# Performance work log

Hardware: AMD Instinct MI355X
Metric: run time of the kernel (lower is better)

## Reference

```python
import jax, jax.numpy as jnp
import numpy as np

N_NODES = 50000
N_EDGES = 800000
DIM = 128


def setup_inputs() -> dict:
    key = jax.random.key(0)
    k_x, k_e, k_w1, k_w2 = jax.random.split(key, 4)
    x = jax.random.normal(k_x, (N_NODES, DIM), dtype=jnp.float32)
    edge_index = jax.random.randint(k_e, (2, N_EDGES), 0, N_NODES, dtype=jnp.int64)
    scale = 1.0 / np.sqrt(DIM)
    W1 = jax.random.normal(k_w1, (DIM, DIM), dtype=jnp.float32) * scale
    b1 = jnp.zeros((DIM,), dtype=jnp.float32)
    W2 = jax.random.normal(k_w2, (DIM, DIM), dtype=jnp.float32) * scale
    b2 = jnp.zeros((DIM,), dtype=jnp.float32)
    return {"x": x, "edge_index": edge_index, "W1": W1, "b1": b1, "W2": W2, "b2": b2}


def _gcn_conv(x, W, b, src, dst, n_nodes):
    """PyG GCNConv: D^{-1/2}(A+I)D^{-1/2} (x @ W) + b, self-loops added."""
    h = x @ W  # [N, D]
    ones = jnp.ones(src.shape[0], dtype=h.dtype)
    # degree of A+I, counting incoming edges at target nodes plus self-loop
    deg = jax.ops.segment_sum(ones, dst, num_segments=n_nodes) + 1.0
    dinv = jax.lax.rsqrt(deg)  # [N]
    norm = dinv[src] * dinv[dst]  # [E]
    msgs = h[src] * norm[:, None]  # [E, D] gather (memory-bound)
    agg = jax.ops.segment_sum(msgs, dst, num_segments=n_nodes)  # scatter-add
    agg = agg + h * (dinv * dinv)[:, None]  # self-loop contribution
    return agg + b


def reference(x, edge_index, W1, b1, W2, b2):
    src, dst = edge_index[0], edge_index[1]
    n = x.shape[0]
    identity = x
    out = jax.nn.relu(_gcn_conv(x, W1, b1, src, dst, n))
    out = _gcn_conv(out, W2, b2, src, dst, n)
    return jax.nn.relu(out + identity)
```

## Files before the change

kernel.cpp:

```cpp
#include <hip/hip_runtime.h>

#define N_NODES 50000
#define N_EDGES 800000
#define DIM 128
#define NB 391
#define CAP 2560
#define NCH 7
#define BIN_CHUNK 4096
#define BIN_BLOCKS 196
#define GEMM_TILES 782
#define AGG_TILES 3125

typedef unsigned int uint;
typedef unsigned short ushort;
typedef __attribute__((ext_vector_type(8))) __bf16 bf16x8;
typedef __attribute__((ext_vector_type(4))) float f32x4;

__device__ __forceinline__ uint f2bf(float f) {
    uint u = __float_as_uint(f);
    return (u + 0x7FFFu + ((u >> 16) & 1u)) >> 16;
}
__device__ __forceinline__ float2 bf2f2(uint u) {
    return make_float2(__uint_as_float(u << 16), __uint_as_float(u & 0xFFFF0000u));
}


__global__ __launch_bounds__(256) void prep_kernel(const float* __restrict__ W1,
                                                   const float* __restrict__ W2,
                                                   uint* __restrict__ Wt1,
                                                   uint* __restrict__ Wt2,
                                                   int* __restrict__ bincursor) {
    int idx = blockIdx.x * 256 + threadIdx.x;
    if (idx < 16384) {
        const float* W = (idx < 8192) ? W1 : W2;
        uint* Wt = (idx < 8192) ? Wt1 : Wt2;
        int i = idx & 8191;
        int n = i >> 6, k2 = i & 63;
        Wt[i] = f2bf(W[(2 * k2) * DIM + n]) | (f2bf(W[(2 * k2 + 1) * DIM + n]) << 16);
    } else {
        int b = idx - 16384;
        if (b < NB) bincursor[b] = b * CAP;
    }
}


__device__ __forceinline__ void gemm_tile64(const float* __restrict__ X,
                                            const uint* __restrict__ Wt, int base,
                                            uint* __restrict__ Hout) {
    int t = threadIdx.x;
    int wv = t >> 6;
    int l = t & 63;
    int col = l & 15;
    int g = l >> 4;
    int grow = base + wv * 16 + col;
    int ar = grow > N_NODES - 1 ? N_NODES - 1 : grow;

    bf16x8 af[4];
    const float4* Xr = (const float4*)(X + (size_t)ar * DIM);
#pragma unroll
    for (int kk = 0; kk < 4; ++kk) {
        float4 x0 = Xr[kk * 8 + g * 2];
        float4 x1 = Xr[kk * 8 + g * 2 + 1];
        uint4 p;
        p.x = f2bf(x0.x) | (f2bf(x0.y) << 16);
        p.y = f2bf(x0.z) | (f2bf(x0.w) << 16);
        p.z = f2bf(x1.x) | (f2bf(x1.y) << 16);
        p.w = f2bf(x1.z) | (f2bf(x1.w) << 16);
        af[kk] = __builtin_bit_cast(bf16x8, p);
    }

    const uint4* Wr = (const uint4*)Wt;
    f32x4 acc[8];
#pragma unroll
    for (int n = 0; n < 8; ++n) acc[n] = (f32x4){0.f, 0.f, 0.f, 0.f};

#pragma unroll
    for (int n = 0; n < 8; ++n) {
        const uint4* wrow = Wr + (size_t)(n * 16 + col) * 16;
#pragma unroll
        for (int kk = 0; kk < 4; ++kk) {
            bf16x8 bf = __builtin_bit_cast(bf16x8, wrow[kk * 4 + g]);
            acc[n] = __builtin_amdgcn_mfma_f32_16x16x32_bf16(af[kk], bf, acc[n], 0, 0, 0);
        }
    }

#pragma unroll
    for (int j = 0; j < 4; ++j) {
        int row = base + wv * 16 + g * 4 + j;
        if (row < N_NODES) {
            ushort* hrow = (ushort*)(Hout + (size_t)row * 64);
#pragma unroll
            for (int n = 0; n < 8; ++n) hrow[n * 16 + col] = (ushort)f2bf(acc[n][j]);
        }
    }
}


__device__ __forceinline__ void gemm_tile16_lds(const uint* __restrict__ sB,
                                                const uint* __restrict__ Wt,
                                                const float* __restrict__ dinv, int base,
                                                uint* __restrict__ Hout) {
    int t = threadIdx.x;
    int wv = t >> 6;
    int l = t & 63;
    int col = l & 15;
    int g = l >> 4;
    int lr = col;

    bf16x8 af[4];
#pragma unroll
    for (int kk = 0; kk < 4; ++kk) {
        int ui = lr * 64 + ((kk * 16 + g * 4) ^ ((lr & 7) << 2));
        af[kk] = __builtin_bit_cast(bf16x8, *(const uint4*)&sB[ui]);
    }

    const uint4* Wr = (const uint4*)Wt;
    f32x4 acc[2];
#pragma unroll
    for (int nn = 0; nn < 2; ++nn) acc[nn] = (f32x4){0.f, 0.f, 0.f, 0.f};

#pragma unroll
    for (int nn = 0; nn < 2; ++nn) {
        int n = wv * 2 + nn;
        const uint4* wrow = Wr + (size_t)(n * 16 + col) * 16;
#pragma unroll
        for (int kk = 0; kk < 4; ++kk) {
            bf16x8 bf = __builtin_bit_cast(bf16x8, wrow[kk * 4 + g]);
            acc[nn] = __builtin_amdgcn_mfma_f32_16x16x32_bf16(af[kk], bf, acc[nn], 0, 0, 0);
        }
    }

#pragma unroll
    for (int j = 0; j < 4; ++j) {
        int row = base + g * 4 + j;
        float di = dinv[row];
        ushort* hrow = (ushort*)(Hout + (size_t)row * 64);
#pragma unroll
        for (int nn = 0; nn < 2; ++nn) {
            int n = wv * 2 + nn;
            hrow[n * 16 + col] = (ushort)f2bf(acc[nn][j] * di);
        }
    }
}


__global__ __launch_bounds__(256) void bin_gemm1_kernel(const int* __restrict__ ei,
                                                        int* __restrict__ bincursor,
                                                        uint* __restrict__ pairs,
                                                        const float* __restrict__ x,
                                                        const uint* __restrict__ Wt1,
                                                        uint* __restrict__ Hs) {
    if (blockIdx.x >= BIN_BLOCKS) {
        gemm_tile64(x, Wt1, (blockIdx.x - BIN_BLOCKS) * 64, Hs);
        return;
    }
    __shared__ int lh[NB];
    __shared__ int lbase[NB];
    int t = threadIdx.x;
    int eb = blockIdx.x * BIN_CHUNK;

    for (int b = t; b < NB; b += 256) lh[b] = 0;
    __syncthreads();

    int s_reg[16], d_reg[16];
#pragma unroll
    for (int i = 0; i < 16; ++i) {
        int e = eb + i * 256 + t;
        if (e < N_EDGES) {
            s_reg[i] = ei[e];
            d_reg[i] = ei[N_EDGES + e];
            atomicAdd(&lh[d_reg[i] >> 7], 1);
        } else {
            d_reg[i] = -1;
        }
    }
    __syncthreads();

    for (int b = t; b < NB; b += 256) {
        int c = lh[b];
        lbase[b] = c ? atomicAdd(&bincursor[b], c) : 0;
    }
    __syncthreads();
    for (int b = t; b < NB; b += 256) lh[b] = 0;
    __syncthreads();

#pragma unroll
    for (int i = 0; i < 16; ++i) {
        int d = d_reg[i];
        if (d >= 0) {
            int bin = d >> 7;
            int r = atomicAdd(&lh[bin], 1);
            pairs[lbase[bin] + r] = ((uint)s_reg[i] << 7) | (uint)(d & 127);
        }
    }
}


__global__ __launch_bounds__(256) void fill2_kernel(const uint* __restrict__ pairs,
                                                    const int* __restrict__ bincursor,
                                                    int* __restrict__ rowbeg,
                                                    int* __restrict__ rowend,
                                                    float* __restrict__ dinv,
                                                    int* __restrict__ csr_src) {
    __shared__ int cnt[128 * 8];
    __shared__ int nsum[128];
    __shared__ int nbase[128];
    int t = threadIdx.x;
    int blk = blockIdx.x;
    int bs = blk * CAP;
    int be = bincursor[blk];

    for (int i = t; i < 128 * 8; i += 256) cnt[i] = 0;
    __syncthreads();

    for (int p = bs + t; p < be; p += 256) {
        uint pr = pairs[p];
        atomicAdd(&cnt[(pr & 127u) * 8 + (pr >> 20)], 1);
    }
    __syncthreads();

    if (t < 128) {
        int s = 0;
#pragma unroll
        for (int c = 0; c < NCH; ++c) s += cnt[t * 8 + c];
        nsum[t] = s;
        nbase[t] = s;
    }
    __syncthreads();
#pragma unroll
    for (int off = 1; off < 128; off <<= 1) {
        int v = (t < 128 && t >= off) ? nbase[t - off] : 0;
        __syncthreads();
        if (t < 128) nbase[t] += v;
        __syncthreads();
    }

    if (t < 128) {
        int ex = nbase[t] - nsum[t];
        int node = blk * 128 + t;
        if (node < N_NODES) {
            rowbeg[node] = bs + ex;
            rowend[node] = bs + nbase[t];
            dinv[node] = rsqrtf((float)nsum[t] + 1.0f);
        }
        int run = ex;
#pragma unroll
        for (int c = 0; c < NCH; ++c) {
            int v = cnt[t * 8 + c];
            cnt[t * 8 + c] = run;
            run += v;
        }
    }
    __syncthreads();

    for (int p = bs + t; p < be; p += 256) {
        uint pr = pairs[p];
        int r = atomicAdd(&cnt[(pr & 127u) * 8 + (pr >> 20)], 1);
        csr_src[bs + r] = (int)(pr >> 7);
    }
}


template <bool DSRC>
__device__ __forceinline__ void agg_node(const int* __restrict__ rowbeg,
                                         const int* __restrict__ rowend,
                                         const int* __restrict__ csr_src,
                                         const uint* __restrict__ Hs,
                                         const float* __restrict__ dinv,
                                         const float* __restrict__ bias, int node, int li,
                                         float r[8]) {
    int beg = rowbeg[node];
    int end = rowend[node];
    float di = dinv[node];

    const uint4* H4 = (const uint4*)Hs;
    float a0, a1, a2, a3, a4, a5, a6, a7;
    {
        uint4 su = H4[(size_t)node * 16 + li];
        float2 v0 = bf2f2(su.x), v1 = bf2f2(su.y), v2 = bf2f2(su.z), v3 = bf2f2(su.w);
        float sf = DSRC ? di : 1.0f;
        a0 = sf * v0.x; a1 = sf * v0.y; a2 = sf * v1.x; a3 = sf * v1.y;
        a4 = sf * v2.x; a5 = sf * v2.y; a6 = sf * v3.x; a7 = sf * v3.y;
    }

#define ADDF8(u, f)                                                               \
    {                                                                             \
        float2 v0 = bf2f2(u.x), v1 = bf2f2(u.y), v2 = bf2f2(u.z), v3 = bf2f2(u.w);\
        a0 += f * v0.x; a1 += f * v0.y; a2 += f * v1.x; a3 += f * v1.y;           \
        a4 += f * v2.x; a5 += f * v2.y; a6 += f * v3.x; a7 += f * v3.y;           \
    }

    int e = beg;
    for (; e + 7 < end; e += 8) {
        int s[8];
#pragma unroll
        for (int i = 0; i < 8; ++i) s[i] = csr_src[e + i];
        uint4 u[8];
#pragma unroll
        for (int i = 0; i < 8; ++i) u[i] = H4[(size_t)s[i] * 16 + li];
        float f[8];
#pragma unroll
        for (int i = 0; i < 8; ++i) f[i] = DSRC ? dinv[s[i]] : 1.0f;
#pragma unroll
        for (int i = 0; i < 8; ++i) ADDF8(u[i], f[i]);
    }
    if (e + 3 < end) {
        int s[4];
#pragma unroll
        for (int i = 0; i < 4; ++i) s[i] = csr_src[e + i];
        uint4 u[4];
#pragma unroll
        for (int i = 0; i < 4; ++i) u[i] = H4[(size_t)s[i] * 16 + li];
        float f[4];
#pragma unroll
        for (int i = 0; i < 4; ++i) f[i] = DSRC ? dinv[s[i]] : 1.0f;
#pragma unroll
        for (int i = 0; i < 4; ++i) ADDF8(u[i], f[i]);
        e += 4;
    }
    for (; e < end; ++e) {
        int s = csr_src[e];
        uint4 u = H4[(size_t)s * 16 + li];
        float f = DSRC ? dinv[s] : 1.0f;
        ADDF8(u, f);
    }
#undef ADDF8

    const float4* B4 = (const float4*)bias;
    float4 bb0 = B4[li * 2], bb1 = B4[li * 2 + 1];
    r[0] = a0 * di + bb0.x; r[1] = a1 * di + bb0.y;
    r[2] = a2 * di + bb0.z; r[3] = a3 * di + bb0.w;
    r[4] = a4 * di + bb1.x; r[5] = a5 * di + bb1.y;
    r[6] = a6 * di + bb1.z; r[7] = a7 * di + bb1.w;
}


__global__ __launch_bounds__(256) void aggemm_kernel(const int* __restrict__ rowbeg,
                                                     const int* __restrict__ rowend,
                                                     const int* __restrict__ csr_src,
                                                     const uint* __restrict__ Hs,
                                                     const float* __restrict__ dinv,
                                                     const float* __restrict__ b1,
                                                     const uint* __restrict__ Wt2,
                                                     uint* __restrict__ Hs2) {
    __shared__ uint sB[16 * 64];
    int t = threadIdx.x;
    int wv = t >> 6;
    int lane = t & 63;
    int grp = lane >> 4;
    int li = lane & 15;
    int base = blockIdx.x * 16;

    {
        int row = wv * 4 + grp;
        int node = base + row;
        float r[8];
        agg_node<true>(rowbeg, rowend, csr_src, Hs, dinv, b1, node, li, r);
        uint4 o;
        o.x = f2bf(fmaxf(r[0], 0.f)) | (f2bf(fmaxf(r[1], 0.f)) << 16);
        o.y = f2bf(fmaxf(r[2], 0.f)) | (f2bf(fmaxf(r[3], 0.f)) << 16);
        o.z = f2bf(fmaxf(r[4], 0.f)) | (f2bf(fmaxf(r[5], 0.f)) << 16);
        o.w = f2bf(fmaxf(r[6], 0.f)) | (f2bf(fmaxf(r[7], 0.f)) << 16);
        int ui = row * 64 + ((li * 4) ^ ((row & 7) << 2));
        *(uint4*)&sB[ui] = o;
    }
    __syncthreads();

    gemm_tile16_lds(sB, Wt2, dinv, base, Hs2);
}


__global__ __launch_bounds__(256) void agg2_kernel(const int* __restrict__ rowbeg,
                                                   const int* __restrict__ rowend,
                                                   const int* __restrict__ csr_src,
                                                   const uint* __restrict__ Hs2,
                                                   const float* __restrict__ dinv,
                                                   const float* __restrict__ b2,
                                                   const float* __restrict__ resid,
                                                   float* __restrict__ out) {
    int wave = (int)((blockIdx.x * (size_t)blockDim.x + threadIdx.x) >> 6);
    int lane = threadIdx.x & 63;
    int grp = lane >> 4;
    int li = lane & 15;
    int node = wave * 4 + grp;

    float r[8];
    agg_node<false>(rowbeg, rowend, csr_src, Hs2, dinv, b2, node, li, r);

    const float4* R4 = (const float4*)(resid + (size_t)node * DIM);
    float4 x0 = R4[li * 2], x1 = R4[li * 2 + 1];
    r[0] += x0.x; r[1] += x0.y; r[2] += x0.z; r[3] += x0.w;
    r[4] += x1.x; r[5] += x1.y; r[6] += x1.z; r[7] += x1.w;

    float4* O4 = (float4*)(out + (size_t)node * DIM);
    O4[li * 2] = make_float4(fmaxf(r[0], 0.f), fmaxf(r[1], 0.f), fmaxf(r[2], 0.f),
                             fmaxf(r[3], 0.f));
    O4[li * 2 + 1] = make_float4(fmaxf(r[4], 0.f), fmaxf(r[5], 0.f), fmaxf(r[6], 0.f),
                                 fmaxf(r[7], 0.f));
}


extern "C" void kernel_launch(void* const* d_in, const int* in_sizes, int n_in,
                              void* d_out, int out_size, void* d_ws, size_t ws_size,
                              hipStream_t stream) {
    const float* x = (const float*)d_in[0];
    const int* edge_index = (const int*)d_in[1];
    const float* W1 = (const float*)d_in[2];
    const float* b1 = (const float*)d_in[3];
    const float* W2 = (const float*)d_in[4];
    const float* b2 = (const float*)d_in[5];
    float* out = (float*)d_out;

    char* ws = (char*)d_ws;
    int*   bincursor = (int*)(ws + 0);
    float* dinv      = (float*)(ws + (64 << 10));
    int*   rowbeg    = (int*)(ws + (320 << 10));
    int*   rowend    = (int*)(ws + (576 << 10));
    int*   csr_src   = (int*)(ws + (1 << 20));
    uint*  pairs     = (uint*)(ws + (6 << 20));
    uint*  Hs        = (uint*)(ws + (11 << 20));
    uint*  Hs2       = (uint*)(ws + (24 << 20));
    uint*  Wt1       = (uint*)(ws + (37 << 20));
    uint*  Wt2       = (uint*)(ws + (37 << 20) + (64 << 10));

    prep_kernel<<<66, 256, 0, stream>>>(W1, W2, Wt1, Wt2, bincursor);
    bin_gemm1_kernel<<<BIN_BLOCKS + GEMM_TILES, 256, 0, stream>>>(edge_index, bincursor, pairs,
                                                                  x, Wt1, Hs);
    fill2_kernel<<<NB, 256, 0, stream>>>(pairs, bincursor, rowbeg, rowend, dinv, csr_src);
    aggemm_kernel<<<AGG_TILES, 256, 0, stream>>>(rowbeg, rowend, csr_src, Hs, dinv, b1, Wt2,
                                                 Hs2);
    agg2_kernel<<<3125, 256, 0, stream>>>(rowbeg, rowend, csr_src, Hs2, dinv, b2, x, out);
}
```

Baseline: 120.9 us.

## Make aggregate+GEMM2 wave-local, removing block barrier with per-wave LDS strips

Each wave now aggregates its own 4 nodes, stages them in a private padded LDS strip, and runs the second GEMM on just those 4 rows (rows replicated across the 16-row MFMA A operand), so the block-wide __syncthreads is gone. Waves no longer wait for the slowest neighbor's irregular-degree aggregation before starting MFMA work. In exchange, each wave does all 8 output column tiles with 4x redundant A rows, loading the full W2 per wave and quadrupling MFMA work, and only a quarter of lanes write results.

Result: slower. 152.3 us (+26.0%).

```diff
diff --git a/kernel.cpp b/kernel.cpp
--- a/kernel.cpp
+++ b/kernel.cpp
@@ -96,54 +96,6 @@
 }
 
 
-__device__ __forceinline__ void gemm_tile16_lds(const uint* __restrict__ sB,
-                                                const uint* __restrict__ Wt,
-                                                const float* __restrict__ dinv, int base,
-                                                uint* __restrict__ Hout) {
-    int t = threadIdx.x;
-    int wv = t >> 6;
-    int l = t & 63;
-    int col = l & 15;
-    int g = l >> 4;
-    int lr = col;
-
-    bf16x8 af[4];
-#pragma unroll
-    for (int kk = 0; kk < 4; ++kk) {
-        int ui = lr * 64 + ((kk * 16 + g * 4) ^ ((lr & 7) << 2));
-        af[kk] = __builtin_bit_cast(bf16x8, *(const uint4*)&sB[ui]);
-    }
-
-    const uint4* Wr = (const uint4*)Wt;
-    f32x4 acc[2];
-#pragma unroll
-    for (int nn = 0; nn < 2; ++nn) acc[nn] = (f32x4){0.f, 0.f, 0.f, 0.f};
-
-#pragma unroll
-    for (int nn = 0; nn < 2; ++nn) {
-        int n = wv * 2 + nn;
-        const uint4* wrow = Wr + (size_t)(n * 16 + col) * 16;
-#pragma unroll
-        for (int kk = 0; kk < 4; ++kk) {
-            bf16x8 bf = __builtin_bit_cast(bf16x8, wrow[kk * 4 + g]);
-            acc[nn] = __builtin_amdgcn_mfma_f32_16x16x32_bf16(af[kk], bf, acc[nn], 0, 0, 0);
-        }
-    }
-
-#pragma unroll
-    for (int j = 0; j < 4; ++j) {
-        int row = base + g * 4 + j;
-        float di = dinv[row];
-        ushort* hrow = (ushort*)(Hout + (size_t)row * 64);
-#pragma unroll
-        for (int nn = 0; nn < 2; ++nn) {
-            int n = wv * 2 + nn;
-            hrow[n * 16 + col] = (ushort)f2bf(acc[nn][j] * di);
-        }
-    }
-}
-
-
 __global__ __launch_bounds__(256) void bin_gemm1_kernel(const int* __restrict__ ei,
                                                         int* __restrict__ bincursor,
                                                         uint* __restrict__ pairs,
@@ -343,30 +295,59 @@
                                                      const float* __restrict__ b1,
                                                      const uint* __restrict__ Wt2,
                                                      uint* __restrict__ Hs2) {
-    __shared__ uint sB[16 * 64];
+    __shared__ uint sB[4][4 * 68];
     int t = threadIdx.x;
     int wv = t >> 6;
     int lane = t & 63;
     int grp = lane >> 4;
     int li = lane & 15;
     int base = blockIdx.x * 16;
-
-    {
-        int row = wv * 4 + grp;
-        int node = base + row;
-        float r[8];
-        agg_node<true>(rowbeg, rowend, csr_src, Hs, dinv, b1, node, li, r);
-        uint4 o;
-        o.x = f2bf(fmaxf(r[0], 0.f)) | (f2bf(fmaxf(r[1], 0.f)) << 16);
-        o.y = f2bf(fmaxf(r[2], 0.f)) | (f2bf(fmaxf(r[3], 0.f)) << 16);
-        o.z = f2bf(fmaxf(r[4], 0.f)) | (f2bf(fmaxf(r[5], 0.f)) << 16);
-        o.w = f2bf(fmaxf(r[6], 0.f)) | (f2bf(fmaxf(r[7], 0.f)) << 16);
-        int ui = row * 64 + ((li * 4) ^ ((row & 7) << 2));
-        *(uint4*)&sB[ui] = o;
-    }
-    __syncthreads();
-
-    gemm_tile16_lds(sB, Wt2, dinv, base, Hs2);
+    int node = base + wv * 4 + grp;
+
+    float r[8];
+    agg_node<true>(rowbeg, rowend, csr_src, Hs, dinv, b1, node, li, r);
+
+    uint4 o;
+    o.x = f2bf(fmaxf(r[0], 0.f)) | (f2bf(fmaxf(r[1], 0.f)) << 16);
+    o.y = f2bf(fmaxf(r[2], 0.f)) | (f2bf(fmaxf(r[3], 0.f)) << 16);
+    o.z = f2bf(fmaxf(r[4], 0.f)) | (f2bf(fmaxf(r[5], 0.f)) << 16);
+    o.w = f2bf(fmaxf(r[6], 0.f)) | (f2bf(fmaxf(r[7], 0.f)) << 16);
+    uint* strip = sB[wv];
+    *(uint4*)&strip[grp * 68 + li * 4] = o;
+    asm volatile("s_waitcnt lgkmcnt(0)" ::: "memory");
+
+    bf16x8 af[4];
+#pragma unroll
+    for (int kk = 0; kk < 4; ++kk) {
+        af[kk] = __builtin_bit_cast(
+            bf16x8, *(const uint4*)&strip[(lane & 3) * 68 + kk * 16 + grp * 4]);
+    }
+
+    float di4[4];
+    if (grp == 0) {
+#pragma unroll
+        for (int j = 0; j < 4; ++j) di4[j] = dinv[base + wv * 4 + j];
+    }
+
+    const uint4* Wr = (const uint4*)Wt2;
+#pragma unroll
+    for (int n = 0; n < 8; ++n) {
+        f32x4 acc = (f32x4){0.f, 0.f, 0.f, 0.f};
+        const uint4* wrow = Wr + (size_t)(n * 16 + li) * 16;
+#pragma unroll
+        for (int kk = 0; kk < 4; ++kk) {
+            bf16x8 bf = __builtin_bit_cast(bf16x8, wrow[kk * 4 + grp]);
+            acc = __builtin_amdgcn_mfma_f32_16x16x32_bf16(af[kk], bf, acc, 0, 0, 0);
+        }
+        if (grp == 0) {
+#pragma unroll
+            for (int j = 0; j < 4; ++j) {
+                int row = base + wv * 4 + j;
+                ((ushort*)(Hs2 + (size_t)row * 64))[n * 16 + li] =
+                    (ushort)f2bf(acc[j] * di4[j]);
+            }
+        }
+    }
 }
 
 
```
